# Performance work log

Hardware: AMD Instinct MI355X
Metric: run time of the kernel (lower is better)

## Reference

```python
import jax, jax.numpy as jnp
import numpy as np
import math
from jax.ops import segment_sum

TOPK_RATIO = 0.1
CLUSTER_RATIO = 0.25
K_KNN = 10


def setup_inputs() -> dict:
    key = jax.random.key(0)
    ks = jax.random.split(key, 10)
    N, C, H, W = 8, 256, 100, 352
    sc = 0.02
    return {
        "spatial_features_2d": jax.random.normal(ks[0], (N, C, H, W), jnp.float32),
        "dis_priority": jax.random.uniform(ks[1], (N, H, W), dtype=jnp.float32),
        "score_w1": jax.random.normal(ks[2], (256, 256), jnp.float32) * sc,
        "score_b1": jnp.zeros((256,), jnp.float32),
        "score_w2": jax.random.normal(ks[3], (1, 256), jnp.float32) * sc,
        "score_b2": jnp.zeros((1,), jnp.float32),
        "cls_w": jax.random.normal(ks[4], (2, 256), jnp.float32) * sc,
        "cls_b": jnp.zeros((2,), jnp.float32),
        "reg_w": jax.random.normal(ks[5], (14, 256), jnp.float32) * sc,
        "reg_b": jnp.zeros((14,), jnp.float32),
        "record_len": jnp.array([2, 3, 1, 2], jnp.int32),
    }


def _forward(x, dis_priority, score_w1, score_b1, score_w2, score_b2,
             cls_w, cls_b, reg_w, reg_b, record_len):
    N, C, H, W = x.shape
    L = H * W
    xf = x.reshape(N, C, L)  # [N,C,L]

    # --- SortSampler: per-pixel 2-layer fc score net (1x1 convs) ---
    h = jax.nn.relu(jnp.einsum('oc,ncl->nol', score_w1, xf) + score_b1[None, :, None])
    scores = jax.nn.sigmoid(jnp.einsum('oc,ncl->nol', score_w2, h) + score_b2[None, :, None])[:, 0]  # [N,L]
    weight = scores * dis_priority.reshape(N, L)
    K = max(int(math.ceil(L * TOPK_RATIO)), 1)  # static topk token count
    sort_idx = jnp.argsort(-weight, axis=1)[:, :K]              # pos_embed [N,K]
    conf = jnp.take_along_axis(weight, sort_idx, axis=1)        # [N,K]
    feats = jnp.take_along_axis(xf, sort_idx[:, None, :], axis=2)  # [N,C,K]
    src = jnp.transpose(feats, (0, 2, 1)) * conf[:, :, None]    # [N,K,C]

    # --- cluster_dpc_knn ---
    M = max(int(math.ceil(K * CLUSTER_RATIO)), 1)
    sq = jnp.sum(src * src, axis=-1)                             # [N,K]
    dist = sq[:, :, None] + sq[:, None, :] - 2.0 * jnp.einsum('nkc,njc->nkj', src, src)
    dist = jnp.maximum(dist, 0.0)                                # [N,K,K]
    dist_nearest = -jax.lax.top_k(-dist, K_KNN)[0]               # [N,K,k] smallest
    density = jnp.exp(-jnp.mean(dist_nearest, axis=-1))          # [N,K]
    density = density + jnp.arange(K, dtype=density.dtype) * 1e-6  # deterministic tie-break
    higher = density[:, None, :] > density[:, :, None]           # [N,K,K]
    dist_max = jnp.max(dist)
    d_higher = jnp.where(higher, dist, dist_max)
    delta = jnp.min(d_higher, axis=-1)                           # [N,K]
    score = delta * density
    idx_centers = jax.lax.top_k(score, M)[1]                     # [N,M]
    # assign each token to nearest cluster center
    dist_centers = jnp.take_along_axis(dist, idx_centers[:, :, None], axis=1)  # [N,M,K]
    idx_cluster = jnp.argmin(dist_centers, axis=1)               # [N,K]
    idx_cluster = idx_cluster.at[jnp.arange(N)[:, None], idx_centers].set(
        jnp.broadcast_to(jnp.arange(M), (N, M)))

    # --- merge_tokens: weighted average per cluster ---
    flat_seg = (idx_cluster + jnp.arange(N, dtype=idx_cluster.dtype)[:, None] * M).reshape(-1)
    w = conf.reshape(-1)
    all_w = segment_sum(w, flat_seg, num_segments=N * M) + 1e-6          # [N*M]
    merged = segment_sum((src * conf[:, :, None]).reshape(N * K, C), flat_seg,
                         num_segments=N * M) / all_w[:, None]
    merged = merged.reshape(N, M, C)
    # index_points: broadcast merged cluster feature back to each token
    src_tok = jnp.take_along_axis(merged, idx_cluster[:, :, None], axis=1)  # [N,K,C]
    src_ct = jnp.transpose(src_tok, (0, 2, 1))                   # [N,C,K]

    # --- scatter tokens back into BEV grid ---
    def scat(idxs, f):  # idxs [K], f [C,K]
        return jnp.zeros((C, L), f.dtype).at[:, idxs].set(f)
    bev = jax.vmap(scat)(sort_idx, src_ct)                       # [N,C,L]
    # ego CAVs (index 0 within each record) keep the full dense feature
    offsets = jnp.concatenate([jnp.zeros((1,), jnp.int32),
                               jnp.cumsum(record_len)[:-1].astype(jnp.int32)])
    is_ego = jnp.any(jnp.arange(N)[:, None] == offsets[None, :], axis=1)  # [N]
    bev = jnp.where(is_ego[:, None, None], xf, bev).reshape(N, C, H, W)

    # --- ego heads (1x1 convs) ---
    ego = x[offsets]                                              # [B,C,H,W]
    psm_ego = jnp.einsum('oc,bchw->bohw', cls_w, ego) + cls_b[None, :, None, None]
    rm_ego = jnp.einsum('oc,bchw->bohw', reg_w, ego) + reg_b[None, :, None, None]
    return bev, psm_ego, rm_ego


def reference(spatial_features_2d, dis_priority, score_w1, score_b1, score_w2, score_b2,
              cls_w, cls_b, reg_w, reg_b, record_len):
    return _forward(spatial_features_2d, dis_priority, score_w1, score_b1, score_w2,
                    score_b2, cls_w, cls_b, reg_w, reg_b, record_len)
```

## Files before the change

### kernel.cpp

```cpp
#include <hip/hip_runtime.h>
#include <hip/hip_bf16.h>

#define CCH   256
#define LPIX  35200
#define KSEL  3520
#define MCL   880
#define NBINS 16384
#define FMAXV 3.402823466e38f

typedef __bf16 bf16x8 __attribute__((ext_vector_type(8)));
typedef float  f32x4  __attribute__((ext_vector_type(4)));
typedef unsigned short ushort_t;

__device__ __forceinline__ void split3(float v, __bf16* h, __bf16* m, __bf16* l) {
    __bf16 a = (__bf16)v;
    float r = v - (float)a;
    __bf16 b = (__bf16)r;
    float r2 = r - (float)b;
    *h = a; *m = b; *l = (__bf16)r2;
}

__device__ constexpr int SA6[6] = {0, 0, 1, 0, 1, 2};
__device__ constexpr int SB6[6] = {0, 1, 0, 2, 1, 0};

__global__ void split_w1(const float* __restrict__ w1, __bf16* __restrict__ h,
                         __bf16* __restrict__ m, __bf16* __restrict__ l) {
    int i = blockIdx.x * 256 + threadIdx.x;
    split3(w1[i], &h[i], &m[i], &l[i]);
}

__global__ __launch_bounds__(256) void score_mfma(
    const float* __restrict__ x, const float* __restrict__ prio,
    const __bf16* __restrict__ w1h, const __bf16* __restrict__ w1m, const __bf16* __restrict__ w1l,
    const float* __restrict__ b1, const float* __restrict__ w2, const float* __restrict__ b2,
    float* __restrict__ weight) {
    int n = blockIdx.y;
    int l0 = blockIdx.x * 64;
    int tid = threadIdx.x, w = tid >> 6, lane = tid & 63;
    int lrow = lane & 15, kg = lane >> 4;
    __shared__ __align__(16) __bf16 Xs[2][3][64][40];
    __shared__ float spart[64][17];
    const float* xb = x + (size_t)n * CCH * LPIX;
    f32x4 acc[4][4];
#pragma unroll
    for (int i = 0; i < 4; i++)
#pragma unroll
        for (int j = 0; j < 4; j++) acc[i][j] = (f32x4){0.f, 0.f, 0.f, 0.f};

    int sl = tid & 63;
    int cg = tid >> 6;

    auto loadx = [&](int k, float* dst) {
        int c0 = k * 32 + cg * 8;
#pragma unroll
        for (int j = 0; j < 8; j++)
            dst[j] = xb[(size_t)(c0 + j) * LPIX + l0 + sl];
    };
    auto loadw = [&](int k, bf16x8* dst) {
#pragma unroll
        for (int fi = 0; fi < 4; fi++) {
            size_t ao = (size_t)(w * 64 + fi * 16 + lrow) * 256 + k * 32 + kg * 8;
            dst[fi * 3 + 0] = *(const bf16x8*)&w1h[ao];
            dst[fi * 3 + 1] = *(const bf16x8*)&w1m[ao];
            dst[fi * 3 + 2] = *(const bf16x8*)&w1l[ao];
        }
    };
    auto stage = [&](int buf, const float* v) {
        bf16x8 vh, vm, vl;
#pragma unroll
        for (int j = 0; j < 8; j++) {
            __bf16 h, m, l;
            split3(v[j], &h, &m, &l);
            vh[j] = h; vm[j] = m; vl[j] = l;
        }
        *(bf16x8*)&Xs[buf][0][sl][cg * 8] = vh;
        *(bf16x8*)&Xs[buf][1][sl][cg * 8] = vm;
        *(bf16x8*)&Xs[buf][2][sl][cg * 8] = vl;
    };

    float pf[2][8];
    bf16x8 wfr[2][12];
    loadx(0, pf[0]);
    loadw(0, wfr[0]);
    stage(0, pf[0]);
    loadx(1, pf[1]);
    __syncthreads();

#pragma unroll
    for (int k = 0; k < 8; k++) {
        const int buf = k & 1;
        bf16x8 bf[3][4];
#pragma unroll
        for (int fj = 0; fj < 4; fj++) {
            bf[0][fj] = *(const bf16x8*)&Xs[buf][0][fj * 16 + lrow][kg * 8];
            bf[1][fj] = *(const bf16x8*)&Xs[buf][1][fj * 16 + lrow][kg * 8];
            bf[2][fj] = *(const bf16x8*)&Xs[buf][2][fj * 16 + lrow][kg * 8];
        }
        if (k < 7) loadw(k + 1, wfr[buf ^ 1]);
        if (k < 6) loadx(k + 2, pf[buf]);
        if (k < 7) stage(buf ^ 1, pf[buf ^ 1]);
#pragma unroll
        for (int t = 0; t < 6; t++) {
#pragma unroll
            for (int fi = 0; fi < 4; fi++) {
#pragma unroll
                for (int fj = 0; fj < 4; fj++) {
                    acc[fi][fj] = __builtin_amdgcn_mfma_f32_16x16x32_bf16(
                        wfr[buf][fi * 3 + SA6[t]], bf[SB6[t]][fj], acc[fi][fj], 0, 0, 0);
                }
            }
        }
        __syncthreads();
    }

    float ps[4] = {0.f, 0.f, 0.f, 0.f};
#pragma unroll
    for (int fi = 0; fi < 4; fi++) {
        int ob = w * 64 + fi * 16 + kg * 4;
        float4 b1v = *(const float4*)&b1[ob];
        float4 w2v = *(const float4*)&w2[ob];
        float b1a[4] = {b1v.x, b1v.y, b1v.z, b1v.w};
        float w2a[4] = {w2v.x, w2v.y, w2v.z, w2v.w};
#pragma unroll
        for (int r = 0; r < 4; r++)
#pragma unroll
            for (int fj = 0; fj < 4; fj++)
                ps[fj] += w2a[r] * fmaxf(acc[fi][fj][r] + b1a[r], 0.f);
    }
#pragma unroll
    for (int fj = 0; fj < 4; fj++) spart[fj * 16 + lrow][w * 4 + kg] = ps[fj];
    __syncthreads();
    if (tid < 64) {
        float s = 0.f;
#pragma unroll
        for (int r = 0; r < 16; r++) s += spart[tid][r];
        s += b2[0];
        float sg = 1.f / (1.f + expf(-s));
        weight[(size_t)n * LPIX + l0 + tid] = sg * prio[(size_t)n * LPIX + l0 + tid];
    }
}

__global__ void hist_kernel(const float* __restrict__ weight, int* __restrict__ hist) {
    int n = blockIdx.y;
    int i = blockIdx.x * 256 + threadIdx.x;
    if (i >= LPIX) return;
    float w = weight[(size_t)n * LPIX + i];
    int b = (int)(w * (float)NBINS);
    b = min(max(b, 0), NBINS - 1);
    atomicAdd(&hist[(size_t)n * NBINS + b], 1);
}

__global__ __launch_bounds__(256) void thr_kernel(const int* __restrict__ hist, int* __restrict__ thrbin) {
    int n = blockIdx.x, t = threadIdx.x;
    const int CH = NBINS / 256;
    __shared__ int csum[256];
    __shared__ int bfound;
    int base = NBINS - (t + 1) * CH;
    int s = 0;
    for (int i = 0; i < CH; i++) s += hist[(size_t)n * NBINS + base + i];
    csum[t] = s;
    __syncthreads();
    if (t == 0) {
        int cum = 0, sel = 255;
        for (int u = 0; u < 256; u++) {
            cum += csum[u];
            csum[u] = cum;
            if (cum >= KSEL) { sel = u; break; }
        }
        bfound = sel;
    }
    __syncthreads();
    if (t == 0) {
        int u = bfound;
        int cumBefore = (u == 0) ? 0 : csum[u - 1];
        int base2 = NBINS - (u + 1) * CH;
        int cum = cumBefore, bsel = base2;
        for (int b = base2 + CH - 1; b >= base2; b--) {
            cum += hist[(size_t)n * NBINS + b];
            if (cum >= KSEL) { bsel = b; break; }
        }
        thrbin[n] = bsel;
    }
}

__global__ void cand_kernel(const float* __restrict__ weight, const int* __restrict__ thrbin,
                            float* __restrict__ candw, int* __restrict__ cidx, int* __restrict__ ccnt) {
    int n = blockIdx.y;
    int i = blockIdx.x * 256 + threadIdx.x;
    if (i >= LPIX) return;
    float w = weight[(size_t)n * LPIX + i];
    int b = (int)(w * (float)NBINS);
    b = min(max(b, 0), NBINS - 1);
    if (b >= thrbin[n]) {
        int p = atomicAdd(&ccnt[n], 1);
        candw[(size_t)n * LPIX + p] = w;
        cidx[(size_t)n * LPIX + p] = i;
    }
}

__global__ __launch_bounds__(256) void rank_kernel(const float* __restrict__ candw, const int* __restrict__ cidx,
                                                   const int* __restrict__ ccnt,
                                                   float* __restrict__ conf, int* __restrict__ sidx) {
    int n = blockIdx.y, i = blockIdx.x;
    int cnt = ccnt[n];
    if (i >= cnt) return;
    float wi = candw[(size_t)n * LPIX + i];
    int ii = cidx[(size_t)n * LPIX + i];
    int r = 0;
    for (int j = threadIdx.x; j < cnt; j += 256) {
        float wj = candw[(size_t)n * LPIX + j];
        int ij = cidx[(size_t)n * LPIX + j];
        if (wj > wi || (wj == wi && ij < ii)) r++;
    }
    __shared__ int red[256];
    red[threadIdx.x] = r;
    __syncthreads();
    for (int s = 128; s > 0; s >>= 1) {
        if (threadIdx.x < s) red[threadIdx.x] += red[threadIdx.x + s];
        __syncthreads();
    }
    if (threadIdx.x == 0) {
        int rank = red[0];
        if (rank < KSEL) {
            sidx[(size_t)n * KSEL + rank] = ii;
            conf[(size_t)n * KSEL + rank] = wi;
        }
    }
}

__global__ __launch_bounds__(256) void gather_src(const float* __restrict__ x, const int* __restrict__ sidx,
                                                  const float* __restrict__ conf,
                                                  float* __restrict__ src,
                                                  __bf16* __restrict__ sh, __bf16* __restrict__ sm,
                                                  __bf16* __restrict__ sl,
                                                  float* __restrict__ sq, int* __restrict__ inv) {
    int n = blockIdx.y, k = blockIdx.x, c = threadIdx.x;
    int idx = sidx[(size_t)n * KSEL + k];
    float cf = conf[(size_t)n * KSEL + k];
    float v = x[((size_t)n * CCH + c) * LPIX + idx] * cf;
    size_t o = ((size_t)n * KSEL + k) * CCH + c;
    src[o] = v;
    __bf16 h, m, l;
    split3(v, &h, &m, &l);
    sh[o] = h; sm[o] = m; sl[o] = l;
    __shared__ float red[256];
    red[c] = v * v;
    __syncthreads();
    for (int s = 128; s > 0; s >>= 1) {
        if (c < s) red[c] += red[c + s];
        __syncthreads();
    }
    if (c == 0) {
        sq[(size_t)n * KSEL + k] = red[0];
        inv[(size_t)n * LPIX + idx] = k;
    }
}

__global__ __launch_bounds__(256) void dist_mfma(
    const __bf16* __restrict__ sh, const __bf16* __restrict__ sm, const __bf16* __restrict__ sl,
    const float* __restrict__ sq, float* __restrict__ dist, int n0) {
    int n = n0 + blockIdx.z;
    const size_t nbase = (size_t)n * KSEL * CCH;
    const float* sqn = sq + (size_t)n * KSEL;
    float* D = dist + (size_t)blockIdx.z * KSEL * KSEL;
    int b = blockIdx.x;
    int iT = (int)((sqrtf(8.f * (float)b + 1.f) - 1.f) * 0.5f);
    while ((iT + 1) * (iT + 2) / 2 <= b) iT++;
    while (iT * (iT + 1) / 2 > b) iT--;
    int jT = b - iT * (iT + 1) / 2;
    int bi = iT * 128, bj = jT * 128;
    __shared__ __align__(16) __bf16 As[3][128][40], Bs[3][128][40];
    int tid = threadIdx.x, w = tid >> 6, lane = tid & 63;
    int lrow = lane & 15, kg = lane >> 4;
    int wr = w >> 1, wc = w & 1;
    f32x4 acc[4][4];
#pragma unroll
    for (int i = 0; i < 4; i++)
#pragma unroll
        for (int j = 0; j < 4; j++) acc[i][j] = (f32x4){0.f, 0.f, 0.f, 0.f};

    int sr = tid & 127, g2 = tid >> 7;
    size_t ra = nbase + (size_t)min(bi + sr, KSEL - 1) * CCH;
    size_t rb = nbase + (size_t)min(bj + sr, KSEL - 1) * CCH;

    bf16x8 rA[3][2], rB[3][2];
#pragma unroll
    for (int s2 = 0; s2 < 2; s2++) {
        int cg = s2 * 2 + g2;
        rA[0][s2] = *(const bf16x8*)&sh[ra + cg * 8];
        rA[1][s2] = *(const bf16x8*)&sm[ra + cg * 8];
        rA[2][s2] = *(const bf16x8*)&sl[ra + cg * 8];
        rB[0][s2] = *(const bf16x8*)&sh[rb + cg * 8];
        rB[1][s2] = *(const bf16x8*)&sm[rb + cg * 8];
        rB[2][s2] = *(const bf16x8*)&sl[rb + cg * 8];
    }
    for (int c0 = 0; c0 < 256; c0 += 32) {
        __syncthreads();
#pragma unroll
        for (int s2 = 0; s2 < 2; s2++) {
            int cg = s2 * 2 + g2;
            *(bf16x8*)&As[0][sr][cg * 8] = rA[0][s2];
            *(bf16x8*)&As[1][sr][cg * 8] = rA[1][s2];
            *(bf16x8*)&As[2][sr][cg * 8] = rA[2][s2];
            *(bf16x8*)&Bs[0][sr][cg * 8] = rB[0][s2];
            *(bf16x8*)&Bs[1][sr][cg * 8] = rB[1][s2];
            *(bf16x8*)&Bs[2][sr][cg * 8] = rB[2][s2];
        }
        __syncthreads();
        if (c0 < 224) {
            int c1 = c0 + 32;
#pragma unroll
            for (int s2 = 0; s2 < 2; s2++) {
                int cg = s2 * 2 + g2;
                rA[0][s2] = *(const bf16x8*)&sh[ra + c1 + cg * 8];
                rA[1][s2] = *(const bf16x8*)&sm[ra + c1 + cg * 8];
                rA[2][s2] = *(const bf16x8*)&sl[ra + c1 + cg * 8];
                rB[0][s2] = *(const bf16x8*)&sh[rb + c1 + cg * 8];
                rB[1][s2] = *(const bf16x8*)&sm[rb + c1 + cg * 8];
                rB[2][s2] = *(const bf16x8*)&sl[rb + c1 + cg * 8];
            }
        }
        bf16x8 af[3][4], bf[3][4];
#pragma unroll
        for (int fj = 0; fj < 4; fj++) {
            int brow = wc * 64 + fj * 16 + lrow;
            bf[0][fj] = *(const bf16x8*)&Bs[0][brow][kg * 8];
            bf[1][fj] = *(const bf16x8*)&Bs[1][brow][kg * 8];
            bf[2][fj] = *(const bf16x8*)&Bs[2][brow][kg * 8];
        }
#pragma unroll
        for (int fi = 0; fi < 4; fi++) {
            int arow = wr * 64 + fi * 16 + lrow;
            af[0][fi] = *(const bf16x8*)&As[0][arow][kg * 8];
            af[1][fi] = *(const bf16x8*)&As[1][arow][kg * 8];
            af[2][fi] = *(const bf16x8*)&As[2][arow][kg * 8];
        }
#pragma unroll
        for (int t = 0; t < 6; t++) {
#pragma unroll
            for (int fi = 0; fi < 4; fi++) {
#pragma unroll
                for (int fj = 0; fj < 4; fj++) {
                    acc[fi][fj] = __builtin_amdgcn_mfma_f32_16x16x32_bf16(
                        af[SA6[t]][fi], bf[SB6[t]][fj], acc[fi][fj], 0, 0, 0);
                }
            }
        }
    }
#pragma unroll
    for (int fi = 0; fi < 4; fi++) {
        int gi0 = bi + wr * 64 + fi * 16;
        if (gi0 >= KSEL) continue;
        float4 siv = *(const float4*)&sqn[gi0 + kg * 4];
        float sia[4] = {siv.x, siv.y, siv.z, siv.w};
#pragma unroll
        for (int fj = 0; fj < 4; fj++) {
            int gj0 = bj + wc * 64 + fj * 16;
            if (gj0 >= KSEL) continue;
            int gj = gj0 + lrow;
            float sj = sqn[gj];
            float dv[4];
#pragma unroll
            for (int r = 0; r < 4; r++) {
                int gi = gi0 + kg * 4 + r;
                dv[r] = fmaxf(sia[r] + sj - 2.f * acc[fi][fj][r], 0.f);
                D[(size_t)gi * KSEL + gj] = dv[r];
            }
            if (iT != jT) {
                *(float4*)&D[(size_t)gj * KSEL + gi0 + kg * 4] = *(float4*)dv;
            }
        }
    }
}

__global__ __launch_bounds__(256) void knn_density(const float* __restrict__ dist, float* __restrict__ density, int n0) {
    int n = n0 + blockIdx.y;
    int row = threadIdx.x >> 6;
    int lane = threadIdx.x & 63;
    int i = blockIdx.x * 4 + row;
    const float4* row4 = (const float4*)(dist + (size_t)blockIdx.y * KSEL * KSEL + (size_t)i * KSEL);
    float tt[10];
#pragma unroll
    for (int r = 0; r < 10; r++) tt[r] = FMAXV;
    for (int j4 = lane; j4 < KSEL / 4; j4 += 64) {
        float4 v4 = row4[j4];
        float vv[4] = {v4.x, v4.y, v4.z, v4.w};
#pragma unroll
        for (int q = 0; q < 4; q++) {
            float v = vv[q];
            if (v < tt[9]) {
                tt[9] = v;
#pragma unroll
                for (int r = 9; r > 0; r--) {
                    if (tt[r] < tt[r - 1]) { float tmp = tt[r - 1]; tt[r - 1] = tt[r]; tt[r] = tmp; }
                }
            }
        }
    }
    __shared__ float ls[4][64][10];
#pragma unroll
    for (int r = 0; r < 10; r++) ls[row][lane][r] = tt[r];
    __syncthreads();
    for (int s = 32; s >= 1; s >>= 1) {
        if (lane < s) {
            float out[10];
            int ia = 0, ib = 0;
#pragma unroll
            for (int r = 0; r < 10; r++) {
                float va = ls[row][lane][ia], vb = ls[row][lane + s][ib];
                if (va <= vb) { out[r] = va; ia++; } else { out[r] = vb; ib++; }
            }
#pragma unroll
            for (int r = 0; r < 10; r++) ls[row][lane][r] = out[r];
        }
        __syncthreads();
    }
    if (lane == 0) {
        float sum = 0.f;
#pragma unroll
        for (int r = 0; r < 10; r++) sum += ls[row][0][r];
        density[(size_t)n * KSEL + i] = expf(-sum * 0.1f) + (float)i * 1e-6f;
    }
}

__global__ __launch_bounds__(256) void delta_score(const float* __restrict__ dist, const float* __restrict__ density,
                                                   float* __restrict__ scoreb, int n0) {
    int n = n0 + blockIdx.y;
    int i = blockIdx.x;
    const float4* row = (const float4*)(dist + (size_t)blockIdx.y * KSEL * KSEL + (size_t)i * KSEL);
    const float* dn = density + (size_t)n * KSEL;
    const float4* dn4 = (const float4*)dn;
    float di = dn[i];
    float mn = FMAXV;
    for (int j4 = threadIdx.x; j4 < KSEL / 4; j4 += 256) {
        float4 d = dn4[j4];
        float4 v = row[j4];
        if (d.x > di) mn = fminf(mn, v.x);
        if (d.y > di) mn = fminf(mn, v.y);
        if (d.z > di) mn = fminf(mn, v.z);
        if (d.w > di) mn = fminf(mn, v.w);
    }
    __shared__ float red[256];
    red[threadIdx.x] = mn;
    __syncthreads();
    for (int s = 128; s > 0; s >>= 1) {
        if (threadIdx.x < s) red[threadIdx.x] = fminf(red[threadIdx.x], red[threadIdx.x + s]);
        __syncthreads();
    }
    if (threadIdx.x == 0) {
        float d = red[0];
        scoreb[(size_t)n * KSEL + i] = (d == FMAXV) ? FMAXV : d * di;
    }
}

__global__ __launch_bounds__(256) void center_rank(const float* __restrict__ scoreb, int* __restrict__ centers,
                                                   int* __restrict__ crank, int n0) {
    int n = n0 + blockIdx.y;
    int i = blockIdx.x;
    const float* sc = scoreb + (size_t)n * KSEL;
    float si = sc[i];
    int r = 0;
    for (int j = threadIdx.x; j < KSEL; j += 256) {
        float sj = sc[j];
        if (sj > si || (sj == si && j < i)) r++;
    }
    __shared__ int red[256];
    red[threadIdx.x] = r;
    __syncthreads();
    for (int s = 128; s > 0; s >>= 1) {
        if (threadIdx.x < s) red[threadIdx.x] += red[threadIdx.x + s];
        __syncthreads();
    }
    if (threadIdx.x == 0) {
        int rank = red[0];
        if (rank < MCL) {
            centers[(size_t)n * MCL + rank] = i;
            crank[(size_t)n * KSEL + i] = rank;
        }
    }
}

__global__ __launch_bounds__(256) void assign_kernel(const float* __restrict__ dist, const int* __restrict__ centers,
                                                     const int* __restrict__ crank, const float* __restrict__ conf,
                                                     int* __restrict__ clus, float* __restrict__ allw, int n0) {
    int n = n0 + blockIdx.y;
    const float* D = dist + (size_t)blockIdx.y * KSEL * KSEL;
    int kl = threadIdx.x & 63, mc = threadIdx.x >> 6;
    int k = blockIdx.x * 64 + kl;
    const int* ctr = centers + (size_t)n * MCL;
    float mn = FMAXV;
    int am = MCL;
    for (int m = mc * 220; m < (mc + 1) * 220; m++) {
        float v = D[(size_t)ctr[m] * KSEL + k];
        if (v < mn) { mn = v; am = m; }
    }
    __shared__ float mv[4][64];
    __shared__ int mi[4][64];
    mv[mc][kl] = mn;
    mi[mc][kl] = am;
    __syncthreads();
    if (mc == 0) {
        float best = mv[0][kl];
        int bm = mi[0][kl];
#pragma unroll
        for (int c = 1; c < 4; c++) {
            float v = mv[c][kl];
            int im = mi[c][kl];
            if (v < best || (v == best && im < bm)) { best = v; bm = im; }
        }
        int cr = crank[(size_t)n * KSEL + k];
        int cl = (cr >= 0) ? cr : bm;
        clus[(size_t)n * KSEL + k] = cl;
        atomicAdd(&allw[(size_t)n * MCL + cl], conf[(size_t)n * KSEL + k]);
    }
}

__global__ void merge_feat(const float* __restrict__ src, const float* __restrict__ conf,
                           const int* __restrict__ clus, float* __restrict__ merged, int n0) {
    int n = n0 + blockIdx.y;
    int k = blockIdx.x, c = threadIdx.x;
    float v = src[((size_t)n * KSEL + k) * CCH + c] * conf[(size_t)n * KSEL + k];
    atomicAdd(&merged[((size_t)n * MCL + clus[(size_t)n * KSEL + k]) * CCH + c], v);
}

__global__ void merged_div(float* __restrict__ merged, const float* __restrict__ allw) {
    int nm = blockIdx.x, c = threadIdx.x;
    merged[(size_t)nm * CCH + c] /= (allw[nm] + 1e-6f);
}

__global__ __launch_bounds__(256) void bev_kernel(const float* __restrict__ x, const int* __restrict__ inv,
                                                  const int* __restrict__ clus, const float* __restrict__ merged,
                                                  const int* __restrict__ reclen, int B,
                                                  const float* __restrict__ clsw, const float* __restrict__ clsb,
                                                  const float* __restrict__ regw, const float* __restrict__ regb,
                                                  float* __restrict__ out, float* __restrict__ psm,
                                                  float* __restrict__ rm) {
    int n = blockIdx.y;
    int l0 = (blockIdx.x * 256 + threadIdx.x) * 4;
    bool ego = false;
    int bego = 0;
    {
        int off = 0;
        for (int b = 0; b < B; b++) {
            if (n == off) { ego = true; bego = b; break; }
            off += reclen[b];
        }
    }
    __shared__ float ws[16][256];
    __shared__ float bs[16];
    if (ego) {
        for (int i = threadIdx.x; i < 16 * 256; i += 256) {
            int o = i >> 8, c = i & 255;
            ws[o][c] = (o < 2) ? clsw[o * 256 + c] : regw[(o - 2) * 256 + c];
        }
        if (threadIdx.x < 16) bs[threadIdx.x] = (threadIdx.x < 2) ? clsb[threadIdx.x] : regb[threadIdx.x - 2];
        __syncthreads();
    }
    if (l0 >= LPIX) return;
    size_t base = (size_t)n * CCH * LPIX + l0;
    if (ego) {
        float acc[16][4] = {};
        for (int c = 0; c < CCH; c++) {
            float4 v = *(const float4*)&x[base + (size_t)c * LPIX];
            *(float4*)&out[base + (size_t)c * LPIX] = v;
#pragma unroll
            for (int o = 0; o < 16; o++) {
                float wv = ws[o][c];
                acc[o][0] += wv * v.x; acc[o][1] += wv * v.y; acc[o][2] += wv * v.z; acc[o][3] += wv * v.w;
            }
        }
#pragma unroll
        for (int o = 0; o < 2; o++) {
            float4 r;
            r.x = acc[o][0] + bs[o]; r.y = acc[o][1] + bs[o]; r.z = acc[o][2] + bs[o]; r.w = acc[o][3] + bs[o];
            *(float4*)&psm[((size_t)bego * 2 + o) * LPIX + l0] = r;
        }
#pragma unroll
        for (int o = 0; o < 14; o++) {
            float4 r;
            float bb = bs[o + 2];
            r.x = acc[o + 2][0] + bb; r.y = acc[o + 2][1] + bb; r.z = acc[o + 2][2] + bb; r.w = acc[o + 2][3] + bb;
            *(float4*)&rm[((size_t)bego * 14 + o) * LPIX + l0] = r;
        }
    } else {
        const float* mr0; const float* mr1; const float* mr2; const float* mr3;
        {
            int t0 = inv[(size_t)n * LPIX + l0 + 0];
            int t1 = inv[(size_t)n * LPIX + l0 + 1];
            int t2 = inv[(size_t)n * LPIX + l0 + 2];
            int t3 = inv[(size_t)n * LPIX + l0 + 3];
            mr0 = (t0 >= 0) ? merged + ((size_t)n * MCL + clus[(size_t)n * KSEL + t0]) * CCH : nullptr;
            mr1 = (t1 >= 0) ? merged + ((size_t)n * MCL + clus[(size_t)n * KSEL + t1]) * CCH : nullptr;
            mr2 = (t2 >= 0) ? merged + ((size_t)n * MCL + clus[(size_t)n * KSEL + t2]) * CCH : nullptr;
            mr3 = (t3 >= 0) ? merged + ((size_t)n * MCL + clus[(size_t)n * KSEL + t3]) * CCH : nullptr;
        }
        for (int c = 0; c < CCH; c++) {
            float4 v;
            v.x = mr0 ? mr0[c] : 0.f;
            v.y = mr1 ? mr1[c] : 0.f;
            v.z = mr2 ? mr2[c] : 0.f;
            v.w = mr3 ? mr3[c] : 0.f;
            *(float4*)&out[base + (size_t)c * LPIX] = v;
        }
    }
}

extern "C" void kernel_launch(void* const* d_in, const int* in_sizes, int n_in,
                              void* d_out, int out_size, void* d_ws, size_t ws_size,
                              hipStream_t stream) {
    const float* x    = (const float*)d_in[0];
    const float* prio = (const float*)d_in[1];
    const float* w1   = (const float*)d_in[2];
    const float* b1   = (const float*)d_in[3];
    const float* w2   = (const float*)d_in[4];
    const float* b2   = (const float*)d_in[5];
    const float* clsw = (const float*)d_in[6];
    const float* clsb = (const float*)d_in[7];
    const float* regw = (const float*)d_in[8];
    const float* regb = (const float*)d_in[9];
    const int* reclen = (const int*)d_in[10];
    int N = in_sizes[0] / (CCH * LPIX);
    int B = in_sizes[10];
    float* out = (float*)d_out;

    char* p = (char*)d_ws;
    size_t off = 0;
    auto alloc = [&](size_t bytes) -> void* {
        void* r = p + off;
        off += (bytes + 255) & ~(size_t)255;
        return r;
    };
    __bf16* w1h    = (__bf16*)alloc(256 * 256 * 2);
    __bf16* w1m    = (__bf16*)alloc(256 * 256 * 2);
    __bf16* w1l    = (__bf16*)alloc(256 * 256 * 2);
    float* weight  = (float*)alloc((size_t)N * LPIX * 4);
    int*   hist    = (int*)alloc((size_t)N * NBINS * 4);
    int*   thrbin  = (int*)alloc((size_t)N * 4);
    int*   ccnt    = (int*)alloc((size_t)N * 4);
    float* candw   = (float*)alloc((size_t)N * LPIX * 4);
    int*   cidx    = (int*)alloc((size_t)N * LPIX * 4);
    int*   sidx    = (int*)alloc((size_t)N * KSEL * 4);
    float* conf    = (float*)alloc((size_t)N * KSEL * 4);
    float* src     = (float*)alloc((size_t)N * KSEL * CCH * 4);
    __bf16* srch   = (__bf16*)alloc((size_t)N * KSEL * CCH * 2);
    __bf16* srcm   = (__bf16*)alloc((size_t)N * KSEL * CCH * 2);
    __bf16* srcl   = (__bf16*)alloc((size_t)N * KSEL * CCH * 2);
    float* sq      = (float*)alloc((size_t)N * KSEL * 4);
    int*   inv     = (int*)alloc((size_t)N * LPIX * 4);
    float* density = (float*)alloc((size_t)N * KSEL * 4);
    float* scoreb  = (float*)alloc((size_t)N * KSEL * 4);
    int*   centers = (int*)alloc((size_t)N * MCL * 4);
    int*   crank   = (int*)alloc((size_t)N * KSEL * 4);
    int*   clus    = (int*)alloc((size_t)N * KSEL * 4);
    float* allw    = (float*)alloc((size_t)N * MCL * 4);
    float* merged  = (float*)alloc((size_t)N * MCL * CCH * 4);
    const size_t distB = (size_t)KSEL * KSEL * 4;
    size_t rem = (ws_size > off) ? (ws_size - off) : 0;
    int nd = (int)(rem / distB);
    if (nd < 1) nd = 1;
    if (nd > N) nd = N;
    if (nd > 4) nd = 4;
    float* dist = (float*)alloc(distB * nd);

    hipMemsetAsync(hist, 0, (size_t)N * NBINS * 4, stream);
    hipMemsetAsync(ccnt, 0, (size_t)N * 4, stream);
    hipMemsetAsync(inv, 0xFF, (size_t)N * LPIX * 4, stream);
    hipMemsetAsync(crank, 0xFF, (size_t)N * KSEL * 4, stream);
    hipMemsetAsync(allw, 0, (size_t)N * MCL * 4, stream);
    hipMemsetAsync(merged, 0, (size_t)N * MCL * CCH * 4, stream);

    split_w1<<<256, 256, 0, stream>>>(w1, w1h, w1m, w1l);
    score_mfma<<<dim3(LPIX / 64, N), 256, 0, stream>>>(x, prio, w1h, w1m, w1l, b1, w2, b2, weight);
    hist_kernel<<<dim3((LPIX + 255) / 256, N), 256, 0, stream>>>(weight, hist);
    thr_kernel<<<N, 256, 0, stream>>>(hist, thrbin);
    cand_kernel<<<dim3((LPIX + 255) / 256, N), 256, 0, stream>>>(weight, thrbin, candw, cidx, ccnt);
    rank_kernel<<<dim3(8192, N), 256, 0, stream>>>(candw, cidx, ccnt, conf, sidx);
    gather_src<<<dim3(KSEL, N), 256, 0, stream>>>(x, sidx, conf, src, srch, srcm, srcl, sq, inv);

    const int TI = (KSEL + 127) / 128;
    const int NT = TI * (TI + 1) / 2;
    for (int g = 0; g < N; g += nd) {
        int nb = (N - g < nd) ? (N - g) : nd;
        dist_mfma<<<dim3(NT, 1, nb), 256, 0, stream>>>(srch, srcm, srcl, sq, dist, g);
        knn_density<<<dim3(KSEL / 4, nb), 256, 0, stream>>>(dist, density, g);
        delta_score<<<dim3(KSEL, nb), 256, 0, stream>>>(dist, density, scoreb, g);
        center_rank<<<dim3(KSEL, nb), 256, 0, stream>>>(scoreb, centers, crank, g);
        assign_kernel<<<dim3(KSEL / 64, nb), 256, 0, stream>>>(dist, centers, crank, conf, clus, allw, g);
        merge_feat<<<dim3(KSEL, nb), 256, 0, stream>>>(src, conf, clus, merged, g);
    }
    merged_div<<<N * MCL, 256, 0, stream>>>(merged, allw);

    float* psm = out + (size_t)N * CCH * LPIX;
    float* rm  = psm + (size_t)B * 2 * LPIX;
    bev_kernel<<<dim3((LPIX / 4 + 255) / 256, N), 256, 0, stream>>>(
        x, inv, clus, merged, reclen, B, clsw, clsb, regw, regb, out, psm, rm);
}
```

Measured before the change: 1.305 ms.

## Load MFMA operands directly from global memory, dropping LDS staging in score and dist kernels

Both the score MLP kernel and the pairwise distance kernel now load their MFMA operand fragments straight from global memory into registers, removing the shared-memory double buffering and the __syncthreads barriers. This is meant to remove LDS write/read traffic and barrier stalls and to raise occupancy by freeing shared memory. The cost is redundant global/L2 reads: each wave re-reads the x columns and the split-feature rows that were previously shared across the block. It also gives up the explicit software prefetch, and the x loads in the score kernel become strided per-lane gathers.

After: 1.466 ms. 12.3% more time.

```diff
diff --git a/kernel.cpp b/kernel.cpp
--- a/kernel.cpp
+++ b/kernel.cpp
@@ -38,67 +38,50 @@
     int l0 = blockIdx.x * 64;
     int tid = threadIdx.x, w = tid >> 6, lane = tid & 63;
     int lrow = lane & 15, kg = lane >> 4;
-    __shared__ __align__(16) __bf16 Xs[2][3][64][40];
     __shared__ float spart[64][17];
-    const float* xb = x + (size_t)n * CCH * LPIX;
+    const float* xb = x + (size_t)n * CCH * LPIX + l0;
     f32x4 acc[4][4];
 #pragma unroll
     for (int i = 0; i < 4; i++)
 #pragma unroll
         for (int j = 0; j < 4; j++) acc[i][j] = (f32x4){0.f, 0.f, 0.f, 0.f};
 
-    int sl = tid & 63;
-    int cg = tid >> 6;
-
-    auto loadx = [&](int k, float* dst) {
-        int c0 = k * 32 + cg * 8;
-#pragma unroll
-        for (int j = 0; j < 8; j++)
-            dst[j] = xb[(size_t)(c0 + j) * LPIX + l0 + sl];
-    };
-    auto loadw = [&](int k, bf16x8* dst) {
+#pragma unroll
+    for (int k = 0; k < 8; k++) {
+        const int c0 = k * 32 + kg * 8;
+        bf16x8 bf[3][4];
+#pragma unroll
+        for (int fp = 0; fp < 2; fp++) {
+            float xv[2][8];
+#pragma unroll
+            for (int q = 0; q < 2; q++) {
+                int pix = (fp * 2 + q) * 16 + lrow;
+#pragma unroll
+                for (int j = 0; j < 8; j++)
+                    xv[q][j] = xb[(size_t)(c0 + j) * LPIX + pix];
+            }
+#pragma unroll
+            for (int q = 0; q < 2; q++) {
+                bf16x8 vh, vm, vl;
+#pragma unroll
+                for (int j = 0; j < 8; j++) {
+                    __bf16 h, m, l;
+                    split3(xv[q][j], &h, &m, &l);
+                    vh[j] = h; vm[j] = m; vl[j] = l;
+                }
+                bf[0][fp * 2 + q] = vh;
+                bf[1][fp * 2 + q] = vm;
+                bf[2][fp * 2 + q] = vl;
+            }
+        }
+        bf16x8 af[3][4];
 #pragma unroll
         for (int fi = 0; fi < 4; fi++) {
-            size_t ao = (size_t)(w * 64 + fi * 16 + lrow) * 256 + k * 32 + kg * 8;
-            dst[fi * 3 + 0] = *(const bf16x8*)&w1h[ao];
-            dst[fi * 3 + 1] = *(const bf16x8*)&w1m[ao];
-            dst[fi * 3 + 2] = *(const bf16x8*)&w1l[ao];
-        }
-    };
-    auto stage = [&](int buf, const float* v) {
-        bf16x8 vh, vm, vl;
-#pragma unroll
-        for (int j = 0; j < 8; j++) {
-            __bf16 h, m, l;
-            split3(v[j], &h, &m, &l);
-            vh[j] = h; vm[j] = m; vl[j] = l;
-        }
-        *(bf16x8*)&Xs[buf][0][sl][cg * 8] = vh;
-        *(bf16x8*)&Xs[buf][1][sl][cg * 8] = vm;
-        *(bf16x8*)&Xs[buf][2][sl][cg * 8] = vl;
-    };
-
-    float pf[2][8];
-    bf16x8 wfr[2][12];
-    loadx(0, pf[0]);
-    loadw(0, wfr[0]);
-    stage(0, pf[0]);
-    loadx(1, pf[1]);
-    __syncthreads();
-
-#pragma unroll
-    for (int k = 0; k < 8; k++) {
-        const int buf = k & 1;
-        bf16x8 bf[3][4];
-#pragma unroll
-        for (int fj = 0; fj < 4; fj++) {
-            bf[0][fj] = *(const bf16x8*)&Xs[buf][0][fj * 16 + lrow][kg * 8];
-            bf[1][fj] = *(const bf16x8*)&Xs[buf][1][fj * 16 + lrow][kg * 8];
-            bf[2][fj] = *(const bf16x8*)&Xs[buf][2][fj * 16 + lrow][kg * 8];
-        }
-        if (k < 7) loadw(k + 1, wfr[buf ^ 1]);
-        if (k < 6) loadx(k + 2, pf[buf]);
-        if (k < 7) stage(buf ^ 1, pf[buf ^ 1]);
+            size_t ao = (size_t)(w * 64 + fi * 16 + lrow) * 256 + c0;
+            af[0][fi] = *(const bf16x8*)&w1h[ao];
+            af[1][fi] = *(const bf16x8*)&w1m[ao];
+            af[2][fi] = *(const bf16x8*)&w1l[ao];
+        }
 #pragma unroll
         for (int t = 0; t < 6; t++) {
 #pragma unroll
@@ -106,11 +89,10 @@
 #pragma unroll
                 for (int fj = 0; fj < 4; fj++) {
                     acc[fi][fj] = __builtin_amdgcn_mfma_f32_16x16x32_bf16(
-                        wfr[buf][fi * 3 + SA6[t]], bf[SB6[t]][fj], acc[fi][fj], 0, 0, 0);
+                        af[SA6[t]][fi], bf[SB6[t]][fj], acc[fi][fj], 0, 0, 0);
                 }
             }
         }
-        __syncthreads();
     }
 
     float ps[4] = {0.f, 0.f, 0.f, 0.f};
@@ -269,7 +251,6 @@
     while (iT * (iT + 1) / 2 > b) iT--;
     int jT = b - iT * (iT + 1) / 2;
     int bi = iT * 128, bj = jT * 128;
-    __shared__ __align__(16) __bf16 As[3][128][40], Bs[3][128][40];
     int tid = threadIdx.x, w = tid >> 6, lane = tid & 63;
     int lrow = lane & 15, kg = lane >> 4;
     int wr = w >> 1, wc = w & 1;
@@ -279,61 +260,25 @@
 #pragma unroll
         for (int j = 0; j < 4; j++) acc[i][j] = (f32x4){0.f, 0.f, 0.f, 0.f};
 
-    int sr = tid & 127, g2 = tid >> 7;
-    size_t ra = nbase + (size_t)min(bi + sr, KSEL - 1) * CCH;
-    size_t rb = nbase + (size_t)min(bj + sr, KSEL - 1) * CCH;
-
-    bf16x8 rA[3][2], rB[3][2];
-#pragma unroll
-    for (int s2 = 0; s2 < 2; s2++) {
-        int cg = s2 * 2 + g2;
-        rA[0][s2] = *(const bf16x8*)&sh[ra + cg * 8];
-        rA[1][s2] = *(const bf16x8*)&sm[ra + cg * 8];
-        rA[2][s2] = *(const bf16x8*)&sl[ra + cg * 8];
-        rB[0][s2] = *(const bf16x8*)&sh[rb + cg * 8];
-        rB[1][s2] = *(const bf16x8*)&sm[rb + cg * 8];
-        rB[2][s2] = *(const bf16x8*)&sl[rb + cg * 8];
-    }
-    for (int c0 = 0; c0 < 256; c0 += 32) {
-        __syncthreads();
-#pragma unroll
-        for (int s2 = 0; s2 < 2; s2++) {
-            int cg = s2 * 2 + g2;
-            *(bf16x8*)&As[0][sr][cg * 8] = rA[0][s2];
-            *(bf16x8*)&As[1][sr][cg * 8] = rA[1][s2];
-            *(bf16x8*)&As[2][sr][cg * 8] = rA[2][s2];
-            *(bf16x8*)&Bs[0][sr][cg * 8] = rB[0][s2];
-            *(bf16x8*)&Bs[1][sr][cg * 8] = rB[1][s2];
-            *(bf16x8*)&Bs[2][sr][cg * 8] = rB[2][s2];
-        }
-        __syncthreads();
-        if (c0 < 224) {
-            int c1 = c0 + 32;
-#pragma unroll
-            for (int s2 = 0; s2 < 2; s2++) {
-                int cg = s2 * 2 + g2;
-                rA[0][s2] = *(const bf16x8*)&sh[ra + c1 + cg * 8];
-                rA[1][s2] = *(const bf16x8*)&sm[ra + c1 + cg * 8];
-                rA[2][s2] = *(const bf16x8*)&sl[ra + c1 + cg * 8];
-                rB[0][s2] = *(const bf16x8*)&sh[rb + c1 + cg * 8];
-                rB[1][s2] = *(const bf16x8*)&sm[rb + c1 + cg * 8];
-                rB[2][s2] = *(const bf16x8*)&sl[rb + c1 + cg * 8];
-            }
-        }
+    size_t aoff[4], boff[4];
+#pragma unroll
+    for (int f = 0; f < 4; f++) {
+        aoff[f] = nbase + (size_t)min(bi + wr * 64 + f * 16 + lrow, KSEL - 1) * CCH + kg * 8;
+        boff[f] = nbase + (size_t)min(bj + wc * 64 + f * 16 + lrow, KSEL - 1) * CCH + kg * 8;
+    }
+
+#pragma unroll
+    for (int k = 0; k < 8; k++) {
+        const int c0 = k * 32;
         bf16x8 af[3][4], bf[3][4];
 #pragma unroll
-        for (int fj = 0; fj < 4; fj++) {
-            int brow = wc * 64 + fj * 16 + lrow;
-            bf[0][fj] = *(const bf16x8*)&Bs[0][brow][kg * 8];
-            bf[1][fj] = *(const bf16x8*)&Bs[1][brow][kg * 8];
-            bf[2][fj] = *(const bf16x8*)&Bs[2][brow][kg * 8];
-        }
-#pragma unroll
-        for (int fi = 0; fi < 4; fi++) {
-            int arow = wr * 64 + fi * 16 + lrow;
-            af[0][fi] = *(const bf16x8*)&As[0][arow][kg * 8];
-            af[1][fi] = *(const bf16x8*)&As[1][arow][kg * 8];
-            af[2][fi] = *(const bf16x8*)&As[2][arow][kg * 8];
+        for (int f = 0; f < 4; f++) {
+            af[0][f] = *(const bf16x8*)&sh[aoff[f] + c0];
+            af[1][f] = *(const bf16x8*)&sm[aoff[f] + c0];
+            af[2][f] = *(const bf16x8*)&sl[aoff[f] + c0];
+            bf[0][f] = *(const bf16x8*)&sh[boff[f] + c0];
+            bf[1][f] = *(const bf16x8*)&sm[boff[f] + c0];
+            bf[2][f] = *(const bf16x8*)&sl[boff[f] + c0];
         }
 #pragma unroll
         for (int t = 0; t < 6; t++) {
```
